# Kernel optimization log

Measured on AMD Instinct MI355X. Metric: run time of the kernel, lower is better.

The kernel has to match this reference:

```python
import jax, jax.numpy as jnp
import numpy as np

B, T, C = 4, 2048, 1024
H = 16
HD = C // H

def setup_inputs() -> dict:
    key = jax.random.key(0)
    k1, k2, k3 = jax.random.split(key, 3)
    x = jax.random.normal(k1, (B, T, C), dtype=jnp.float32)
    w_attn = jax.random.normal(k2, (C, 3 * C), dtype=jnp.float32) * 0.02
    b_attn = jnp.zeros((3 * C,), dtype=jnp.float32)
    w_proj = jax.random.normal(k3, (C, C), dtype=jnp.float32) * 0.02
    b_proj = jnp.zeros((C,), dtype=jnp.float32)
    return {"x": x, "w_attn": w_attn, "b_attn": b_attn, "w_proj": w_proj, "b_proj": b_proj}

def reference(x, w_attn, b_attn, w_proj, b_proj):
    Bx, Tx, Cx = x.shape
    qkv = x @ w_attn + b_attn                      # [B,T,3C]
    q, k, v = jnp.split(qkv, 3, axis=-1)
    # [B,T,C] -> [B,H,T,HD]
    q = q.reshape(Bx, Tx, H, HD).transpose(0, 2, 1, 3)
    k = k.reshape(Bx, Tx, H, HD).transpose(0, 2, 1, 3)
    v = v.reshape(Bx, Tx, H, HD).transpose(0, 2, 1, 3)
    scale = 1.0 / jnp.sqrt(jnp.asarray(HD, dtype=x.dtype))
    att = jnp.einsum('bhqd,bhkd->bhqk', q, k) * scale
    causal = jnp.tril(jnp.ones((Tx, Tx), dtype=bool))
    att = jnp.where(causal[None, None], att, jnp.finfo(att.dtype).min)
    att = jax.nn.softmax(att, axis=-1)
    y = jnp.einsum('bhqk,bhkd->bhqd', att, v)       # [B,H,T,HD]
    y = y.transpose(0, 2, 1, 3).reshape(Bx, Tx, Cx)
    return y @ w_proj + b_proj
```

## Files before the change

### kernel.cpp

```cpp
#include <hip/hip_runtime.h>
#include <hip/hip_bf16.h>

#define B_ 4
#define T_ 2048
#define C_ 1024
#define H_ 16
#define HD_ 64
#define BT_ (B_*T_)
#define C3_ (3*C_)
#define BHTD_ ((size_t)B_*H_*T_*HD_)

#define QSCALE 0.18033688011112042f

using u16 = unsigned short;
using u32 = unsigned int;
using bf16x8 = __attribute__((ext_vector_type(8))) short;
using f32x4  = __attribute__((ext_vector_type(4))) float;
using f32x16 = __attribute__((ext_vector_type(16))) float;
using u16x4  = __attribute__((ext_vector_type(4))) u16;
typedef int i32x2 __attribute__((ext_vector_type(2)));

#if __has_builtin(__builtin_amdgcn_exp2f)
#define EXP2(x) __builtin_amdgcn_exp2f(x)
#else
#define EXP2(x) exp2f(x)
#endif

__device__ __forceinline__ u16 f2bf(float f) {
  u32 u = __float_as_uint(f);
  u += 0x7fffu + ((u >> 16) & 1u);
  return (u16)(u >> 16);
}

__device__ __forceinline__ u32 cvtpk(float lo, float hi) {
  u32 r;
  asm("v_cvt_pk_bf16_f32 %0, %1, %2" : "=v"(r) : "v"(lo), "v"(hi));
  return r;
}

__device__ __forceinline__ void plswap(u32 &a, u32 &b) {
#if __has_builtin(__builtin_amdgcn_permlane32_swap)
  i32x2 r = __builtin_amdgcn_permlane32_swap((int)a, (int)b, false, false);
  a = (u32)r[0]; b = (u32)r[1];
#else
  asm volatile("v_permlane32_swap_b32 %0, %1" : "+v"(a), "+v"(b));
#endif
}

__device__ __forceinline__ float xmaxf(float x) {
  u32 a = __float_as_uint(x), b = a;
  plswap(a, b);
  return fmaxf(__uint_as_float(a), __uint_as_float(b));
}
__device__ __forceinline__ float xaddf(float x) {
  u32 a = __float_as_uint(x), b = a;
  plswap(a, b);
  return __uint_as_float(a) + __uint_as_float(b);
}

__device__ __forceinline__ void gload16(const void* g,
                                        __attribute__((address_space(3))) void* l) {
  __builtin_amdgcn_global_load_lds((const __attribute__((address_space(1))) void*)g,
                                   l, 16, 0, 0);
}

__global__ __launch_bounds__(256) void k_cvt_bf16(const float* __restrict__ in,
                                                  u16* __restrict__ out) {
  size_t i = (size_t)(blockIdx.x * blockDim.x + threadIdx.x) * 4;
  f32x4 f = *(const f32x4*)(in + i);
  u16x4 o;
  o[0] = f2bf(f[0]); o[1] = f2bf(f[1]); o[2] = f2bf(f[2]); o[3] = f2bf(f[3]);
  *(u16x4*)(out + i) = o;
}

__global__ __launch_bounds__(256) void k_transpose_bf16(const float* __restrict__ w,
                                                        u16* __restrict__ wt,
                                                        int K, int N) {
  __shared__ float t[32][33];
  int n0 = blockIdx.x * 32, k0 = blockIdx.y * 32;
  int tx = threadIdx.x & 31;
  int ty = threadIdx.x >> 5;
  #pragma unroll
  for (int r = 0; r < 4; ++r)
    t[ty + r*8][tx] = w[(size_t)(k0 + ty + r*8) * N + n0 + tx];
  __syncthreads();
  #pragma unroll
  for (int r = 0; r < 4; ++r)
    wt[(size_t)(n0 + ty + r*8) * K + k0 + tx] = f2bf(t[tx][ty + r*8]);
}

__global__ __launch_bounds__(256) void k_transpose_v(const u16* __restrict__ src,
                                                     u16* __restrict__ dst) {
  __shared__ u16 t[64][72];
  int bh = blockIdx.y;
  int t0 = blockIdx.x * 64;
  const u16* s = src + (size_t)bh * T_ * HD_;
  u16* d = dst + (size_t)bh * HD_ * T_;
  int r = threadIdx.x >> 2, c0 = (threadIdx.x & 3) * 16;
  bf16x8 a0 = *(const bf16x8*)(s + (size_t)(t0 + r)*HD_ + c0);
  bf16x8 a1 = *(const bf16x8*)(s + (size_t)(t0 + r)*HD_ + c0 + 8);
  #pragma unroll
  for (int j = 0; j < 8; ++j) t[r][c0 + j] = (u16)a0[j];
  #pragma unroll
  for (int j = 0; j < 8; ++j) t[r][c0 + 8 + j] = (u16)a1[j];
  __syncthreads();
  bf16x8 b0, b1;
  #pragma unroll
  for (int j = 0; j < 8; ++j) b0[j] = (short)t[c0 + j][r];
  #pragma unroll
  for (int j = 0; j < 8; ++j) b1[j] = (short)t[c0 + 8 + j][r];
  *(bf16x8*)(d + (size_t)r*T_ + t0 + c0) = b0;
  *(bf16x8*)(d + (size_t)r*T_ + t0 + c0 + 8) = b1;
}

template<int EPI>
__global__ __launch_bounds__(256) void k_gemm(const u16* __restrict__ A,
                                              const u16* __restrict__ Bt,
                                              const float* __restrict__ bias,
                                              void* __restrict__ outp,
                                              void* __restrict__ outp2,
                                              int K) {
  __shared__ __align__(16) u16 lA[128*32];
  __shared__ __align__(16) u16 lB[128*32];
  int tid = threadIdx.x;
  int wave = tid >> 6, lane = tid & 63;
  int wr = wave >> 1, wc = wave & 1;
  int lrow = lane & 15, lgrp = lane >> 4;
  int nwg = gridDim.x * gridDim.y;
  int bidf = blockIdx.y * gridDim.x + blockIdx.x;
  int swzb = (bidf & 7) * (nwg >> 3) + (bidf >> 3);
  int bx = swzb % gridDim.x, by = swzb / gridDim.x;
  int row0 = by * 128, col0 = bx * 128;

  f32x4 zero = {0.f, 0.f, 0.f, 0.f};
  f32x4 acc[4][4];
  #pragma unroll
  for (int m = 0; m < 4; ++m)
    #pragma unroll
    for (int n = 0; n < 4; ++n) acc[m][n] = zero;

  for (int kt = 0; kt < K; kt += 32) {
    #pragma unroll
    for (int p = 0; p < 2; ++p) {
      int c = (wave*2 + p)*64 + lane;
      int r = c >> 2, kc = c & 3;
      int sk = kc ^ ((r >> 1) & 3);
      gload16(A  + (size_t)(row0 + r)*K + kt + sk*8,
              (__attribute__((address_space(3))) char*)lA + (wave*2 + p)*1024);
      gload16(Bt + (size_t)(col0 + r)*K + kt + sk*8,
              (__attribute__((address_space(3))) char*)lB + (wave*2 + p)*1024);
    }
    __syncthreads();
    bf16x8 af[4], bfr[4];
    #pragma unroll
    for (int m = 0; m < 4; ++m) {
      int row = wr*64 + m*16 + lrow;
      af[m] = *(const bf16x8*)(lA + row*32 + (lgrp ^ ((row >> 1) & 3))*8);
    }
    #pragma unroll
    for (int n = 0; n < 4; ++n) {
      int row = wc*64 + n*16 + lrow;
      bfr[n] = *(const bf16x8*)(lB + row*32 + (lgrp ^ ((row >> 1) & 3))*8);
    }
    #pragma unroll
    for (int m = 0; m < 4; ++m)
      #pragma unroll
      for (int n = 0; n < 4; ++n)
        acc[m][n] = __builtin_amdgcn_mfma_f32_16x16x32_bf16(af[m], bfr[n], acc[m][n], 0, 0, 0);
    __syncthreads();
  }

  #pragma unroll
  for (int m = 0; m < 4; ++m) {
    #pragma unroll
    for (int n = 0; n < 4; ++n) {
      int gcol = col0 + wc*64 + n*16 + lrow;
      float bv = bias[gcol];
      #pragma unroll
      for (int r = 0; r < 4; ++r) {
        int grow = row0 + wr*64 + m*16 + lgrp*4 + r;
        float val = acc[m][n][r] + bv;
        if (EPI == 0) {
          int which = gcol >> 10, c = gcol & 1023;
          int hh = c >> 6, d = c & 63;
          int bb = grow >> 11, tt = grow & 2047;
          if (which == 0) val *= QSCALE;
          size_t idx = ((size_t)(bb*H_ + hh)*T_ + tt)*HD_ + d;
          if (which == 2)
            ((u16*)outp2)[idx] = f2bf(val);
          else
            ((u16*)outp)[(size_t)which*BHTD_ + idx] = f2bf(val);
        } else {
          ((float*)outp)[(size_t)grow*C_ + gcol] = val;
        }
      }
    }
  }
}

__global__ __launch_bounds__(256, 2) void k_attn(const u16* __restrict__ q,
                                                 const u16* __restrict__ k,
                                                 const u16* __restrict__ vt,
                                                 u16* __restrict__ y) {
  int tid = threadIdx.x;
  int wave = tid >> 6, lane = tid & 63;
  int l31 = lane & 31, hi = lane >> 5;
  int bid = blockIdx.x;
  int head = bid & 63;
  int g = bid >> 6;
  int s = (g < 4) ? (g*4 + wave) : (31 - (g - 4)*4 - wave);
  int bidx = head >> 4, hh = head & 15;
  const u16* qb = q  + (size_t)head * T_ * HD_;
  const u16* kb = k  + (size_t)head * T_ * HD_;
  const u16* vb = vt + (size_t)head * HD_ * T_;

  f32x16 zero16 = {0.f,0.f,0.f,0.f,0.f,0.f,0.f,0.f,0.f,0.f,0.f,0.f,0.f,0.f,0.f,0.f};

  int qr0 = s * 64;
  bf16x8 qfA[4], qfB[4];
  {
    const u16* qrowA = qb + (size_t)(qr0 + l31)*HD_ + hi*8;
    const u16* qrowB = qrowA + 32*HD_;
    #pragma unroll
    for (int i = 0; i < 4; ++i) { qfA[i] = *(const bf16x8*)(qrowA + 16*i);
                                  qfB[i] = *(const bf16x8*)(qrowB + 16*i); }
  }

  f32x16 oA0 = zero16, oA1 = zero16, oB0 = zero16, oB1 = zero16;
  float mrunA = -1e30f, lrunA = 0.f, mrunB = -1e30f, lrunB = 0.f;
  int qgA = qr0 + l31, qgB = qr0 + 32 + l31;

  auto halfstep = [&](bf16x8 (&qf)[4], f32x16 &od0, f32x16 &od1,
                      float &mrun, float &lrun, int qg, int kv0, bool domask,
                      bf16x8 (&kf)[8], bf16x8 (&vf)[8]) {
    f32x16 s0 = zero16, s1 = zero16;
    __builtin_amdgcn_s_setprio(1);
    s0 = __builtin_amdgcn_mfma_f32_32x32x16_bf16(kf[0], qf[0], s0, 0, 0, 0);
    s1 = __builtin_amdgcn_mfma_f32_32x32x16_bf16(kf[4], qf[0], s1, 0, 0, 0);
    s0 = __builtin_amdgcn_mfma_f32_32x32x16_bf16(kf[1], qf[1], s0, 0, 0, 0);
    s1 = __builtin_amdgcn_mfma_f32_32x32x16_bf16(kf[5], qf[1], s1, 0, 0, 0);
    s0 = __builtin_amdgcn_mfma_f32_32x32x16_bf16(kf[2], qf[2], s0, 0, 0, 0);
    s1 = __builtin_amdgcn_mfma_f32_32x32x16_bf16(kf[6], qf[2], s1, 0, 0, 0);
    s0 = __builtin_amdgcn_mfma_f32_32x32x16_bf16(kf[3], qf[3], s0, 0, 0, 0);
    s1 = __builtin_amdgcn_mfma_f32_32x32x16_bf16(kf[7], qf[3], s1, 0, 0, 0);
    __builtin_amdgcn_s_setprio(0);

    if (domask) {
      #pragma unroll
      for (int r = 0; r < 16; ++r) {
        int kl = (r & 3) + 8*(r >> 2) + 4*hi;
        if (kv0 + kl      > qg) s0[r] = -1e30f;
        if (kv0 + 32 + kl > qg) s1[r] = -1e30f;
      }
    }

    float t[16];
    #pragma unroll
    for (int i = 0; i < 16; ++i) t[i] = fmaxf(s0[i], s1[i]);
    #pragma unroll
    for (int off = 8; off > 0; off >>= 1)
      #pragma unroll
      for (int i = 0; i < 8; ++i)
        if (i < off) t[i] = fmaxf(t[i], t[i + off]);
    float pmax = xmaxf(t[0]);

    if (!__all(pmax <= mrun)) {
      float mnew = fmaxf(mrun, pmax);
      float ex = EXP2(mrun - mnew);
      mrun = mnew;
      lrun *= ex;
      #pragma unroll
      for (int i = 0; i < 16; ++i) { od0[i] *= ex; od1[i] *= ex; }
    }

    #pragma unroll
    for (int i = 0; i < 16; ++i) s0[i] = EXP2(s0[i] - mrun);
    #pragma unroll
    for (int i = 0; i < 16; ++i) s1[i] = EXP2(s1[i] - mrun);
    float u[16];
    #pragma unroll
    for (int i = 0; i < 16; ++i) u[i] = s0[i] + s1[i];
    #pragma unroll
    for (int off = 8; off > 0; off >>= 1)
      #pragma unroll
      for (int i = 0; i < 8; ++i)
        if (i < off) u[i] = u[i] + u[i + off];
    float rsum = xaddf(u[0]);
    lrun += rsum;

    bf16x8 pf0, pf1, pf2, pf3;
    {
      u32 a0 = cvtpk(s0[0], s0[1]),   a1 = cvtpk(s0[2], s0[3]);
      u32 b0 = cvtpk(s0[4], s0[5]),   b1 = cvtpk(s0[6], s0[7]);
      plswap(a0, b0); plswap(a1, b1);
      u32 wa[4] = {a0, a1, b0, b1};
      __builtin_memcpy(&pf0, wa, 16);
    }
    {
      u32 a0 = cvtpk(s0[8], s0[9]),   a1 = cvtpk(s0[10], s0[11]);
      u32 b0 = cvtpk(s0[12], s0[13]), b1 = cvtpk(s0[14], s0[15]);
      plswap(a0, b0); plswap(a1, b1);
      u32 wa[4] = {a0, a1, b0, b1};
      __builtin_memcpy(&pf1, wa, 16);
    }
    {
      u32 a0 = cvtpk(s1[0], s1[1]),   a1 = cvtpk(s1[2], s1[3]);
      u32 b0 = cvtpk(s1[4], s1[5]),   b1 = cvtpk(s1[6], s1[7]);
      plswap(a0, b0); plswap(a1, b1);
      u32 wa[4] = {a0, a1, b0, b1};
      __builtin_memcpy(&pf2, wa, 16);
    }
    {
      u32 a0 = cvtpk(s1[8], s1[9]),   a1 = cvtpk(s1[10], s1[11]);
      u32 b0 = cvtpk(s1[12], s1[13]), b1 = cvtpk(s1[14], s1[15]);
      plswap(a0, b0); plswap(a1, b1);
      u32 wa[4] = {a0, a1, b0, b1};
      __builtin_memcpy(&pf3, wa, 16);
    }

    __builtin_amdgcn_s_setprio(1);
    od0 = __builtin_amdgcn_mfma_f32_32x32x16_bf16(vf[0], pf0, od0, 0, 0, 0);
    od0 = __builtin_amdgcn_mfma_f32_32x32x16_bf16(vf[1], pf1, od0, 0, 0, 0);
    od0 = __builtin_amdgcn_mfma_f32_32x32x16_bf16(vf[2], pf2, od0, 0, 0, 0);
    od0 = __builtin_amdgcn_mfma_f32_32x32x16_bf16(vf[3], pf3, od0, 0, 0, 0);
    od1 = __builtin_amdgcn_mfma_f32_32x32x16_bf16(vf[4], pf0, od1, 0, 0, 0);
    od1 = __builtin_amdgcn_mfma_f32_32x32x16_bf16(vf[5], pf1, od1, 0, 0, 0);
    od1 = __builtin_amdgcn_mfma_f32_32x32x16_bf16(vf[6], pf2, od1, 0, 0, 0);
    od1 = __builtin_amdgcn_mfma_f32_32x32x16_bf16(vf[7], pf3, od1, 0, 0, 0);
    __builtin_amdgcn_s_setprio(0);
  };

  for (int t = 0; t <= s; ++t) {
    int kv0 = t*64;
    bool last = (t == s);

    bf16x8 kf[8], vf[8];
    {
      const u16* krow = kb + (size_t)(kv0 + l31)*HD_ + hi*8;
      const u16* krow1 = krow + 32*HD_;
      #pragma unroll
      for (int i = 0; i < 4; ++i) { kf[i] = *(const bf16x8*)(krow + 16*i);
                                    kf[4+i] = *(const bf16x8*)(krow1 + 16*i); }
      const u16* vrow = vb + (size_t)l31*T_ + kv0 + hi*8;
      const u16* vrow1 = vrow + 32*T_;
      #pragma unroll
      for (int i = 0; i < 4; ++i) { vf[i] = *(const bf16x8*)(vrow + 16*i);
                                    vf[4+i] = *(const bf16x8*)(vrow1 + 16*i); }
    }

    halfstep(qfA, oA0, oA1, mrunA, lrunA, qgA, kv0, last, kf, vf);
    halfstep(qfB, oB0, oB1, mrunB, lrunB, qgB, kv0, last, kf, vf);
  }

  {
    float inv = 1.0f / lrunA;
    u16* yrow = y + ((size_t)(bidx*T_) + qr0 + l31)*C_ + hh*64;
    #pragma unroll
    for (int r = 0; r < 8; ++r) {
      int dp = ((2*r) & 3) + 8*(r >> 1) + 4*hi;
      *(u32*)(yrow + dp)      = cvtpk(oA0[2*r]*inv, oA0[2*r+1]*inv);
      *(u32*)(yrow + 32 + dp) = cvtpk(oA1[2*r]*inv, oA1[2*r+1]*inv);
    }
  }
  {
    float inv = 1.0f / lrunB;
    u16* yrow = y + ((size_t)(bidx*T_) + qr0 + 32 + l31)*C_ + hh*64;
    #pragma unroll
    for (int r = 0; r < 8; ++r) {
      int dp = ((2*r) & 3) + 8*(r >> 1) + 4*hi;
      *(u32*)(yrow + dp)      = cvtpk(oB0[2*r]*inv, oB0[2*r+1]*inv);
      *(u32*)(yrow + 32 + dp) = cvtpk(oB1[2*r]*inv, oB1[2*r+1]*inv);
    }
  }
}

extern "C" void kernel_launch(void* const* d_in, const int* in_sizes, int n_in,
                              void* d_out, int out_size, void* d_ws, size_t ws_size,
                              hipStream_t stream) {
  const float* x      = (const float*)d_in[0];
  const float* w_attn = (const float*)d_in[1];
  const float* b_attn = (const float*)d_in[2];
  const float* w_proj = (const float*)d_in[3];
  const float* b_proj = (const float*)d_in[4];

  char* ws = (char*)d_ws;
  size_t off = 0;
  auto walloc = [&](size_t bytes) -> void* {
    void* p = ws + off;
    off += (bytes + 255) & ~(size_t)255;
    return p;
  };
  u16* xbf  = (u16*)walloc((size_t)BT_ * C_ * 2);
  u16* wat  = (u16*)walloc((size_t)C3_ * C_ * 2);
  u16* wpt  = (u16*)walloc((size_t)C_ * C_ * 2);
  u16* qkv  = (u16*)walloc(3 * BHTD_ * 2);
  u16* vtmp = (u16*)walloc(BHTD_ * 2);
  u16* qp = qkv;
  u16* kp = qkv + BHTD_;
  u16* vp = qkv + 2*BHTD_;
  u16* ybf = xbf;

  k_cvt_bf16<<<(BT_*C_)/1024, 256, 0, stream>>>(x, xbf);
  k_transpose_bf16<<<dim3(C3_/32, C_/32), 256, 0, stream>>>(w_attn, wat, C_, C3_);
  k_transpose_bf16<<<dim3(C_/32, C_/32), 256, 0, stream>>>(w_proj, wpt, C_, C_);
  k_gemm<0><<<dim3(C3_/128, BT_/128), 256, 0, stream>>>(xbf, wat, b_attn, (void*)qkv, (void*)vtmp, C_);
  k_transpose_v<<<dim3(T_/64, B_*H_), 256, 0, stream>>>(vtmp, vp);
  k_attn<<<dim3(512), 256, 0, stream>>>(qp, kp, vp, ybf);
  k_gemm<1><<<dim3(C_/128, BT_/128), 256, 0, stream>>>(ybf, wpt, b_proj, d_out, nullptr, C_);
}
```

Before: 195.2 us.

## Stage K/V tiles in double-buffered LDS shared across waves with paired query tiles

```diff
diff --git a/kernel.cpp b/kernel.cpp
--- a/kernel.cpp
+++ b/kernel.cpp
@@ -202,176 +202,186 @@
                                                  const u16* __restrict__ k,
                                                  const u16* __restrict__ vt,
                                                  u16* __restrict__ y) {
+  __shared__ __align__(16) u16 Kl[2][64][72];
+  __shared__ __align__(16) u16 Vl[2][64][72];
   int tid = threadIdx.x;
   int wave = tid >> 6, lane = tid & 63;
   int l31 = lane & 31, hi = lane >> 5;
   int bid = blockIdx.x;
   int head = bid & 63;
-  int g = bid >> 6;
-  int s = (g < 4) ? (g*4 + wave) : (31 - (g - 4)*4 - wave);
+  int jA = bid >> 6;
   int bidx = head >> 4, hh = head & 15;
   const u16* qb = q  + (size_t)head * T_ * HD_;
   const u16* kb = k  + (size_t)head * T_ * HD_;
   const u16* vb = vt + (size_t)head * HD_ * T_;
 
+  int sr = tid >> 2;
+  int sc = (tid & 3) * 16;
+
   f32x16 zero16 = {0.f,0.f,0.f,0.f,0.f,0.f,0.f,0.f,0.f,0.f,0.f,0.f,0.f,0.f,0.f,0.f};
 
-  int qr0 = s * 64;
-  bf16x8 qfA[4], qfB[4];
-  {
-    const u16* qrowA = qb + (size_t)(qr0 + l31)*HD_ + hi*8;
-    const u16* qrowB = qrowA + 32*HD_;
-    #pragma unroll
-    for (int i = 0; i < 4; ++i) { qfA[i] = *(const bf16x8*)(qrowA + 16*i);
-                                  qfB[i] = *(const bf16x8*)(qrowB + 16*i); }
-  }
-
-  f32x16 oA0 = zero16, oA1 = zero16, oB0 = zero16, oB1 = zero16;
-  float mrunA = -1e30f, lrunA = 0.f, mrunB = -1e30f, lrunB = 0.f;
-  int qgA = qr0 + l31, qgB = qr0 + 32 + l31;
-
-  auto halfstep = [&](bf16x8 (&qf)[4], f32x16 &od0, f32x16 &od1,
-                      float &mrun, float &lrun, int qg, int kv0, bool domask,
-                      bf16x8 (&kf)[8], bf16x8 (&vf)[8]) {
-    f32x16 s0 = zero16, s1 = zero16;
-    __builtin_amdgcn_s_setprio(1);
-    s0 = __builtin_amdgcn_mfma_f32_32x32x16_bf16(kf[0], qf[0], s0, 0, 0, 0);
-    s1 = __builtin_amdgcn_mfma_f32_32x32x16_bf16(kf[4], qf[0], s1, 0, 0, 0);
-    s0 = __builtin_amdgcn_mfma_f32_32x32x16_bf16(kf[1], qf[1], s0, 0, 0, 0);
-    s1 = __builtin_amdgcn_mfma_f32_32x32x16_bf16(kf[5], qf[1], s1, 0, 0, 0);
-    s0 = __builtin_amdgcn_mfma_f32_32x32x16_bf16(kf[2], qf[2], s0, 0, 0, 0);
-    s1 = __builtin_amdgcn_mfma_f32_32x32x16_bf16(kf[6], qf[2], s1, 0, 0, 0);
-    s0 = __builtin_amdgcn_mfma_f32_32x32x16_bf16(kf[3], qf[3], s0, 0, 0, 0);
-    s1 = __builtin_amdgcn_mfma_f32_32x32x16_bf16(kf[7], qf[3], s1, 0, 0, 0);
-    __builtin_amdgcn_s_setprio(0);
-
-    if (domask) {
+  auto runqt = [&](int j) {
+    int qr0 = j*128 + wave*32;
+    bf16x8 qf[4];
+    {
+      const u16* qrow = qb + (size_t)(qr0 + l31)*HD_ + hi*8;
       #pragma unroll
-      for (int r = 0; r < 16; ++r) {
-        int kl = (r & 3) + 8*(r >> 2) + 4*hi;
-        if (kv0 + kl      > qg) s0[r] = -1e30f;
-        if (kv0 + 32 + kl > qg) s1[r] = -1e30f;
+      for (int i = 0; i < 4; ++i) qf[i] = *(const bf16x8*)(qrow + 16*i);
+    }
+    f32x16 od0 = zero16, od1 = zero16;
+    float mrun = -1e30f, lrun = 0.f;
+    int qg = qr0 + l31;
+    int nt = 2*j + 2;
+
+    {
+      const u16* ks = kb + (size_t)sr*HD_ + sc;
+      const u16* vs = vb + (size_t)sr*T_ + sc;
+      bf16x8 k0 = *(const bf16x8*)ks, k1 = *(const bf16x8*)(ks + 8);
+      bf16x8 v0 = *(const bf16x8*)vs, v1 = *(const bf16x8*)(vs + 8);
+      *(bf16x8*)&Kl[0][sr][sc] = k0; *(bf16x8*)&Kl[0][sr][sc + 8] = k1;
+      *(bf16x8*)&Vl[0][sr][sc] = v0; *(bf16x8*)&Vl[0][sr][sc + 8] = v1;
+      __syncthreads();
+    }
+
+    for (int t = 0; t < nt; ++t) {
+      int kv0 = t*64;
+      int cb = t & 1, nb = cb ^ 1;
+      bool haveNext = (t + 1 < nt);
+
+      bf16x8 nk0, nk1, nv0, nv1;
+      if (haveNext) {
+        const u16* ks = kb + (size_t)(kv0 + 64 + sr)*HD_ + sc;
+        const u16* vs = vb + (size_t)sr*T_ + (kv0 + 64) + sc;
+        nk0 = *(const bf16x8*)ks; nk1 = *(const bf16x8*)(ks + 8);
+        nv0 = *(const bf16x8*)vs; nv1 = *(const bf16x8*)(vs + 8);
       }
-    }
-
-    float t[16];
-    #pragma unroll
-    for (int i = 0; i < 16; ++i) t[i] = fmaxf(s0[i], s1[i]);
-    #pragma unroll
-    for (int off = 8; off > 0; off >>= 1)
-      #pragma unroll
-      for (int i = 0; i < 8; ++i)
-        if (i < off) t[i] = fmaxf(t[i], t[i + off]);
-    float pmax = xmaxf(t[0]);
-
-    if (!__all(pmax <= mrun)) {
-      float mnew = fmaxf(mrun, pmax);
-      float ex = EXP2(mrun - mnew);
-      mrun = mnew;
-      lrun *= ex;
-      #pragma unroll
-      for (int i = 0; i < 16; ++i) { od0[i] *= ex; od1[i] *= ex; }
-    }
-
-    #pragma unroll
-    for (int i = 0; i < 16; ++i) s0[i] = EXP2(s0[i] - mrun);
-    #pragma unroll
-    for (int i = 0; i < 16; ++i) s1[i] = EXP2(s1[i] - mrun);
-    float u[16];
-    #pragma unroll
-    for (int i = 0; i < 16; ++i) u[i] = s0[i] + s1[i];
-    #pragma unroll
-    for (int off = 8; off > 0; off >>= 1)
-      #pragma unroll
-      for (int i = 0; i < 8; ++i)
-        if (i < off) u[i] = u[i] + u[i + off];
-    float rsum = xaddf(u[0]);
-    lrun += rsum;
-
-    bf16x8 pf0, pf1, pf2, pf3;
-    {
-      u32 a0 = cvtpk(s0[0], s0[1]),   a1 = cvtpk(s0[2], s0[3]);
-      u32 b0 = cvtpk(s0[4], s0[5]),   b1 = cvtpk(s0[6], s0[7]);
-      plswap(a0, b0); plswap(a1, b1);
-      u32 wa[4] = {a0, a1, b0, b1};
-      __builtin_memcpy(&pf0, wa, 16);
-    }
-    {
-      u32 a0 = cvtpk(s0[8], s0[9]),   a1 = cvtpk(s0[10], s0[11]);
-      u32 b0 = cvtpk(s0[12], s0[13]), b1 = cvtpk(s0[14], s0[15]);
-      plswap(a0, b0); plswap(a1, b1);
-      u32 wa[4] = {a0, a1, b0, b1};
-      __builtin_memcpy(&pf1, wa, 16);
-    }
-    {
-      u32 a0 = cvtpk(s1[0], s1[1]),   a1 = cvtpk(s1[2], s1[3]);
-      u32 b0 = cvtpk(s1[4], s1[5]),   b1 = cvtpk(s1[6], s1[7]);
-      plswap(a0, b0); plswap(a1, b1);
-      u32 wa[4] = {a0, a1, b0, b1};
-      __builtin_memcpy(&pf2, wa, 16);
-    }
-    {
-      u32 a0 = cvtpk(s1[8], s1[9]),   a1 = cvtpk(s1[10], s1[11]);
-      u32 b0 = cvtpk(s1[12], s1[13]), b1 = cvtpk(s1[14], s1[15]);
-      plswap(a0, b0); plswap(a1, b1);
-      u32 wa[4] = {a0, a1, b0, b1};
-      __builtin_memcpy(&pf3, wa, 16);
-    }
-
-    __builtin_amdgcn_s_setprio(1);
-    od0 = __builtin_amdgcn_mfma_f32_32x32x16_bf16(vf[0], pf0, od0, 0, 0, 0);
-    od0 = __builtin_amdgcn_mfma_f32_32x32x16_bf16(vf[1], pf1, od0, 0, 0, 0);
-    od0 = __builtin_amdgcn_mfma_f32_32x32x16_bf16(vf[2], pf2, od0, 0, 0, 0);
-    od0 = __builtin_amdgcn_mfma_f32_32x32x16_bf16(vf[3], pf3, od0, 0, 0, 0);
-    od1 = __builtin_amdgcn_mfma_f32_32x32x16_bf16(vf[4], pf0, od1, 0, 0, 0);
-    od1 = __builtin_amdgcn_mfma_f32_32x32x16_bf16(vf[5], pf1, od1, 0, 0, 0);
-    od1 = __builtin_amdgcn_mfma_f32_32x32x16_bf16(vf[6], pf2, od1, 0, 0, 0);
-    od1 = __builtin_amdgcn_mfma_f32_32x32x16_bf16(vf[7], pf3, od1, 0, 0, 0);
-    __builtin_amdgcn_s_setprio(0);
-  };
-
-  for (int t = 0; t <= s; ++t) {
-    int kv0 = t*64;
-    bool last = (t == s);
-
-    bf16x8 kf[8], vf[8];
-    {
-      const u16* krow = kb + (size_t)(kv0 + l31)*HD_ + hi*8;
-      const u16* krow1 = krow + 32*HD_;
-      #pragma unroll
-      for (int i = 0; i < 4; ++i) { kf[i] = *(const bf16x8*)(krow + 16*i);
-                                    kf[4+i] = *(const bf16x8*)(krow1 + 16*i); }
-      const u16* vrow = vb + (size_t)l31*T_ + kv0 + hi*8;
-      const u16* vrow1 = vrow + 32*T_;
-      #pragma unroll
-      for (int i = 0; i < 4; ++i) { vf[i] = *(const bf16x8*)(vrow + 16*i);
-                                    vf[4+i] = *(const bf16x8*)(vrow1 + 16*i); }
-    }
-
-    halfstep(qfA, oA0, oA1, mrunA, lrunA, qgA, kv0, last, kf, vf);
-    halfstep(qfB, oB0, oB1, mrunB, lrunB, qgB, kv0, last, kf, vf);
-  }
-
-  {
-    float inv = 1.0f / lrunA;
+
+      if (kv0 <= qr0 + 31) {
+        bf16x8 kf[8], vf[8];
+        #pragma unroll
+        for (int i = 0; i < 4; ++i) {
+          int cc = 16*i + 8*hi;
+          kf[i]     = *(const bf16x8*)&Kl[cb][l31][cc];
+          kf[4 + i] = *(const bf16x8*)&Kl[cb][l31 + 32][cc];
+          vf[i]     = *(const bf16x8*)&Vl[cb][l31][cc];
+          vf[4 + i] = *(const bf16x8*)&Vl[cb][l31 + 32][cc];
+        }
+
+        f32x16 s0 = zero16, s1 = zero16;
+        __builtin_amdgcn_s_setprio(1);
+        s0 = __builtin_amdgcn_mfma_f32_32x32x16_bf16(kf[0], qf[0], s0, 0, 0, 0);
+        s1 = __builtin_amdgcn_mfma_f32_32x32x16_bf16(kf[4], qf[0], s1, 0, 0, 0);
+        s0 = __builtin_amdgcn_mfma_f32_32x32x16_bf16(kf[1], qf[1], s0, 0, 0, 0);
+        s1 = __builtin_amdgcn_mfma_f32_32x32x16_bf16(kf[5], qf[1], s1, 0, 0, 0);
+        s0 = __builtin_amdgcn_mfma_f32_32x32x16_bf16(kf[2], qf[2], s0, 0, 0, 0);
+        s1 = __builtin_amdgcn_mfma_f32_32x32x16_bf16(kf[6], qf[2], s1, 0, 0, 0);
+        s0 = __builtin_amdgcn_mfma_f32_32x32x16_bf16(kf[3], qf[3], s0, 0, 0, 0);
+        s1 = __builtin_amdgcn_mfma_f32_32x32x16_bf16(kf[7], qf[3], s1, 0, 0, 0);
+        __builtin_amdgcn_s_setprio(0);
+
+        if (kv0 + 63 > qr0) {
+          #pragma unroll
+          for (int r = 0; r < 16; ++r) {
+            int kl2 = (r & 3) + 8*(r >> 2) + 4*hi;
+            if (kv0 + kl2      > qg) s0[r] = -1e30f;
+            if (kv0 + 32 + kl2 > qg) s1[r] = -1e30f;
+          }
+        }
+
+        float tmx[16];
+        #pragma unroll
+        for (int i = 0; i < 16; ++i) tmx[i] = fmaxf(s0[i], s1[i]);
+        #pragma unroll
+        for (int off = 8; off > 0; off >>= 1)
+          #pragma unroll
+          for (int i = 0; i < 8; ++i)
+            if (i < off) tmx[i] = fmaxf(tmx[i], tmx[i + off]);
+        float pmax = xmaxf(tmx[0]);
+
+        if (!__all(pmax <= mrun)) {
+          float mnew = fmaxf(mrun, pmax);
+          float ex = EXP2(mrun - mnew);
+          mrun = mnew;
+          lrun *= ex;
+          #pragma unroll
+          for (int i = 0; i < 16; ++i) { od0[i] *= ex; od1[i] *= ex; }
+        }
+
+        #pragma unroll
+        for (int i = 0; i < 16; ++i) s0[i] = EXP2(s0[i] - mrun);
+        #pragma unroll
+        for (int i = 0; i < 16; ++i) s1[i] = EXP2(s1[i] - mrun);
+        float u[16];
+        #pragma unroll
+        for (int i = 0; i < 16; ++i) u[i] = s0[i] + s1[i];
+        #pragma unroll
+        for (int off = 8; off > 0; off >>= 1)
+          #pragma unroll
+          for (int i = 0; i < 8; ++i)
+            if (i < off) u[i] = u[i] + u[i + off];
+        lrun += xaddf(u[0]);
+
+        bf16x8 pf0, pf1, pf2, pf3;
+        {
+          u32 a0 = cvtpk(s0[0], s0[1]),   a1 = cvtpk(s0[2], s0[3]);
+          u32 b0 = cvtpk(s0[4], s0[5]),   b1 = cvtpk(s0[6], s0[7]);
+          plswap(a0, b0); plswap(a1, b1);
+          u32 wa[4] = {a0, a1, b0, b1};
+          __builtin_memcpy(&pf0, wa, 16);
+        }
+        {
+          u32 a0 = cvtpk(s0[8], s0[9]),   a1 = cvtpk(s0[10], s0[11]);
+          u32 b0 = cvtpk(s0[12], s0[13]), b1 = cvtpk(s0[14], s0[15]);
+          plswap(a0, b0); plswap(a1, b1);
+          u32 wa[4] = {a0, a1, b0, b1};
+          __builtin_memcpy(&pf1, wa, 16);
+        }
+        {
+          u32 a0 = cvtpk(s1[0], s1[1]),   a1 = cvtpk(s1[2], s1[3]);
+          u32 b0 = cvtpk(s1[4], s1[5]),   b1 = cvtpk(s1[6], s1[7]);
+          plswap(a0, b0); plswap(a1, b1);
+          u32 wa[4] = {a0, a1, b0, b1};
+          __builtin_memcpy(&pf2, wa, 16);
+        }
+        {
+          u32 a0 = cvtpk(s1[8], s1[9]),   a1 = cvtpk(s1[10], s1[11]);
+          u32 b0 = cvtpk(s1[12], s1[13]), b1 = cvtpk(s1[14], s1[15]);
+          plswap(a0, b0); plswap(a1, b1);
+          u32 wa[4] = {a0, a1, b0, b1};
+          __builtin_memcpy(&pf3, wa, 16);
+        }
+
+        __builtin_amdgcn_s_setprio(1);
+        od0 = __builtin_amdgcn_mfma_f32_32x32x16_bf16(vf[0], pf0, od0, 0, 0, 0);
+        od0 = __builtin_amdgcn_mfma_f32_32x32x16_bf16(vf[1], pf1, od0, 0, 0, 0);
+        od0 = __builtin_amdgcn_mfma_f32_32x32x16_bf16(vf[2], pf2, od0, 0, 0, 0);
+        od0 = __builtin_amdgcn_mfma_f32_32x32x16_bf16(vf[3], pf3, od0, 0, 0, 0);
+        od1 = __builtin_amdgcn_mfma_f32_32x32x16_bf16(vf[4], pf0, od1, 0, 0, 0);
+        od1 = __builtin_amdgcn_mfma_f32_32x32x16_bf16(vf[5], pf1, od1, 0, 0, 0);
+        od1 = __builtin_amdgcn_mfma_f32_32x32x16_bf16(vf[6], pf2, od1, 0, 0, 0);
+        od1 = __builtin_amdgcn_mfma_f32_32x32x16_bf16(vf[7], pf3, od1, 0, 0, 0);
+        __builtin_amdgcn_s_setprio(0);
+      }
+
+      if (haveNext) {
+        *(bf16x8*)&Kl[nb][sr][sc] = nk0; *(bf16x8*)&Kl[nb][sr][sc + 8] = nk1;
+        *(bf16x8*)&Vl[nb][sr][sc] = nv0; *(bf16x8*)&Vl[nb][sr][sc + 8] = nv1;
+      }
+      __syncthreads();
+    }
+
+    float inv = 1.0f / lrun;
     u16* yrow = y + ((size_t)(bidx*T_) + qr0 + l31)*C_ + hh*64;
     #pragma unroll
     for (int r = 0; r < 8; ++r) {
       int dp = ((2*r) & 3) + 8*(r >> 1) + 4*hi;
-      *(u32*)(yrow + dp)      = cvtpk(oA0[2*r]*inv, oA0[2*r+1]*inv);
-      *(u32*)(yrow + 32 + dp) = cvtpk(oA1[2*r]*inv, oA1[2*r+1]*inv);
-    }
-  }
-  {
-    float inv = 1.0f / lrunB;
-    u16* yrow = y + ((size_t)(bidx*T_) + qr0 + 32 + l31)*C_ + hh*64;
-    #pragma unroll
-    for (int r = 0; r < 8; ++r) {
-      int dp = ((2*r) & 3) + 8*(r >> 1) + 4*hi;
-      *(u32*)(yrow + dp)      = cvtpk(oB0[2*r]*inv, oB0[2*r+1]*inv);
-      *(u32*)(yrow + 32 + dp) = cvtpk(oB1[2*r]*inv, oB1[2*r+1]*inv);
-    }
-  }
+      *(u32*)(yrow + dp)      = cvtpk(od0[2*r]*inv, od0[2*r+1]*inv);
+      *(u32*)(yrow + 32 + dp) = cvtpk(od1[2*r]*inv, od1[2*r+1]*inv);
+    }
+  };
+
+  runqt(jA);
+  runqt(15 - jA);
 }
 
 extern "C" void kernel_launch(void* const* d_in, const int* in_sizes, int n_in,
```

New measurement: 185.8 us. 1.05x faster.
